# Kernel tuning notes

Hardware: AMD Instinct MI355X
Metric: run time of the kernel (lower is better)

## Reference

```python
import jax, jax.numpy as jnp
import numpy as np

B, T, I, R, O = 128, 512, 64, 512, 64

def setup_inputs() -> dict:
    key = jax.random.key(0)
    ks = jax.random.split(key, 6)
    s = lambda fan_in: 1.0 / np.sqrt(fan_in)
    return {
        "x_pred": jax.random.normal(ks[0], (B, T, I), dtype=jnp.float32),
        "h0": jnp.zeros((B, R), dtype=jnp.float32),
        "W_h": jax.random.uniform(ks[1], (R, R), jnp.float32, -s(R), s(R)),
        "b_h": jax.random.uniform(ks[2], (R,), jnp.float32, -s(R), s(R)),
        "U_h": jax.random.uniform(ks[3], (R, I), jnp.float32, -s(I), s(I)),
        "W_out": jax.random.uniform(ks[4], (O, R), jnp.float32, -s(R), s(R)),
        "b_out": jax.random.uniform(ks[5], (O,), jnp.float32, -s(R), s(R)),
    }

def reference(x_pred, h0, W_h, b_h, U_h, W_out, b_out):
    # Precompute input projections for all timesteps: [T, B, R]
    u = jnp.einsum('bti,ri->tbr', x_pred, U_h)

    def step(x, u_t):
        # x: [B, R] hidden state; u_t: [B, R]
        x = jnp.tanh(x @ W_h.T + b_h + u_t)
        y_t = x @ W_out.T + b_out  # [B, O]
        return x, y_t

    x_last, y = jax.lax.scan(step, h0, u)
    y = jnp.transpose(y, (1, 0, 2))  # [B, T, O]
    return y, (x_last, x_last)
```

## Files before the change

### kernel.cpp

```cpp
#include <hip/hip_runtime.h>

#define B_ 128
#define T_ 512
#define I_ 64
#define R_ 512
#define O_ 64
#define NG 8
#define GB 16

typedef _Float16 f16;
typedef __attribute__((ext_vector_type(8))) _Float16 half8;
typedef __attribute__((ext_vector_type(2))) __fp16 fp16x2;
typedef __attribute__((ext_vector_type(4))) float f32x4;

#define MFMA16 __builtin_amdgcn_mfma_f32_16x16x32_f16

#define NLW 15
#define NRW 49
#define WLDS_BYTES (8 * NLW * 1024)
#define HOFF WLDS_BYTES
#define HBYTES 16384
#define SMEM_TOTAL (WLDS_BYTES + 2 * HBYTES)

__device__ __forceinline__ float tanh_fast(float x) {
    float e = __builtin_amdgcn_exp2f(x * 2.885390081777927f);
    return 1.0f - 2.0f * __builtin_amdgcn_rcpf(e + 1.0f);
}

__device__ __forceinline__ half8 cvt_h8(const float4 a, const float4 b) {
    half8 r;
    r[0] = (f16)a.x; r[1] = (f16)a.y; r[2] = (f16)a.z; r[3] = (f16)a.w;
    r[4] = (f16)b.x; r[5] = (f16)b.y; r[6] = (f16)b.z; r[7] = (f16)b.w;
    return r;
}

__device__ __forceinline__ unsigned pack2(float a, float b) {
    union { fp16x2 h; unsigned u; } r;
    r.h = __builtin_amdgcn_cvt_pkrtz(a, b);
    return r.u;
}

__global__ void __launch_bounds__(256) pre_kernel(
    const float* __restrict__ x_pred, const float* __restrict__ b_h,
    const float* __restrict__ U_h, f16* __restrict__ ubuf)
{
    const int tid = threadIdx.x;
    const int w = tid >> 6, l = tid & 63, lg = l >> 4, ln = l & 15;
    const int g = blockIdx.x & 7, tc = blockIdx.x >> 3;
    const int b0 = g * GB;

    half8 uf[8][2];
    float4 bh4[8];
    #pragma unroll
    for (int j = 0; j < 8; ++j) {
        const int rt = 128 * w + 16 * j;
        bh4[j] = *(const float4*)(b_h + rt + 4 * lg);
        #pragma unroll
        for (int ks = 0; ks < 2; ++ks) {
            const float* p = U_h + (size_t)(rt + ln) * I_ + 32 * ks + 8 * lg;
            uf[j][ks] = cvt_h8(*(const float4*)p, *(const float4*)(p + 4));
        }
    }
    for (int tt = 0; tt < 4; ++tt) {
        const int t = tc * 4 + tt;
        half8 xf[2];
        #pragma unroll
        for (int ks = 0; ks < 2; ++ks) {
            const float* p = x_pred + ((size_t)(b0 + ln) * T_ + t) * I_ + 32 * ks + 8 * lg;
            xf[ks] = cvt_h8(*(const float4*)p, *(const float4*)(p + 4));
        }
        char* ut = (char*)ubuf + (size_t)(t * NG + g) * 16384;
        #pragma unroll
        for (int j = 0; j < 8; ++j) {
            f32x4 acc = {0.f, 0.f, 0.f, 0.f};
            acc = MFMA16(uf[j][0], xf[0], acc, 0, 0, 0);
            acc = MFMA16(uf[j][1], xf[1], acc, 0, 0, 0);
            const int rt = 128 * w + 16 * j;
            uint2 pk;
            pk.x = pack2(acc[0] + bh4[j].x, acc[1] + bh4[j].y);
            pk.y = pack2(acc[2] + bh4[j].z, acc[3] + bh4[j].w);
            *(uint2*)(ut + ln * 1024 + 2 * (rt + 4 * lg)) = pk;
        }
    }
}

__global__ void __launch_bounds__(512, 2) rnn_kernel(
    const float* __restrict__ h0, const float* __restrict__ W_h,
    f16* __restrict__ uh, float* __restrict__ out)
{
    extern __shared__ char smem[];
    const int tid = threadIdx.x;
    const int w = tid >> 6, l = tid & 63, lg = l >> 4, ln = l & 15;
    const int g = blockIdx.x;
    const int b0 = g * GB;
    const int rw = w * 64;
    char* wlds = smem + ((w * NLW) << 10) + (l << 4);

    half8 wfr[NRW];
    #pragma unroll
    for (int j = 0; j < 4; ++j) {
        const float* wr = W_h + (size_t)(rw + 16 * j + ln) * R_;
        #pragma unroll
        for (int ks = 0; ks < 16; ++ks) {
            const float* p = wr + 32 * ks + 8 * lg;
            half8 f = cvt_h8(*(const float4*)p, *(const float4*)(p + 4));
            const int fi = ks * 4 + j;
            if (fi < NLW) *(half8*)(wlds + (fi << 10)) = f;
            else wfr[fi - NLW] = f;
        }
    }
    {
        const int b = tid >> 5, r0 = (tid & 31) * 16;
        const int sb = (b & 7) << 4;
        const float* hp = h0 + (size_t)(b0 + b) * R_ + r0;
        #pragma unroll
        for (int q = 0; q < 4; ++q) {
            float4 v = *(const float4*)(hp + 4 * q);
            uint2 pk;
            pk.x = pack2(v.x, v.y); pk.y = pack2(v.z, v.w);
            *(uint2*)(smem + HOFF + b * 1024 + ((2 * (r0 + 4 * q)) ^ sb)) = pk;
        }
    }
    uint2 uu[4];
    #pragma unroll
    for (int j = 0; j < 4; ++j)
        uu[j] = *(const uint2*)((char*)uh + (size_t)g * 16384 + ln * 1024 + 2 * (rw + 16 * j + 4 * lg));
    __syncthreads();

    const int asb = (ln & 7) << 4;
    const unsigned lanebase = (unsigned)(ln * 1024)
                            + (((unsigned)(16 * lg)) ^ ((unsigned)(ln & 3) << 4))
                            + (((unsigned)(ln >> 2) & 1u) << 6);

    #pragma unroll 1
    for (int t = 0; t < T_; ++t) {
        char* hc = smem + HOFF + (t & 1) * HBYTES;
        char* hn = smem + HOFF + ((t & 1) ^ 1) * HBYTES;
        const char* hbE = hc + lanebase;
        const char* hbO = hc + (lanebase ^ 64u);
        char* slot = (char*)uh + (size_t)(t * NG + g) * 16384;
        const bool lastt = (t == T_ - 1);

        f32x4 acc[4];
        #pragma unroll
        for (int j = 0; j < 4; ++j) {
            union { uint2 u; f16 h[4]; } c; c.u = uu[j];
            acc[j] = (f32x4){(float)c.h[0], (float)c.h[1], (float)c.h[2], (float)c.h[3]};
        }
        if (!lastt) {
            const char* un = (const char*)uh + (size_t)((t + 1) * NG + g) * 16384;
            #pragma unroll
            for (int j = 0; j < 4; ++j)
                uu[j] = *(const uint2*)(un + ln * 1024 + 2 * (rw + 16 * j + 4 * lg));
        }
        __builtin_amdgcn_s_setprio(1);
        #pragma unroll
        for (int ks = 0; ks < 16; ++ks) {
            half8 hb = *(const half8*)((ks & 1 ? hbO : hbE) + 128 * (ks >> 1));
            #pragma unroll
            for (int j = 0; j < 4; ++j) {
                const int fi = ks * 4 + j;
                half8 aa;
                if (fi < NLW) aa = *(const half8*)(wlds + (fi << 10));
                else aa = wfr[fi - NLW];
                acc[j] = MFMA16(aa, hb, acc[j], 0, 0, 0);
            }
        }
        __builtin_amdgcn_s_setprio(0);
        #pragma unroll
        for (int j = 0; j < 4; ++j) {
            const int rb = 2 * (rw + 16 * j + 4 * lg);
            float v0 = tanh_fast(acc[j][0]), v1 = tanh_fast(acc[j][1]);
            float v2 = tanh_fast(acc[j][2]), v3 = tanh_fast(acc[j][3]);
            uint2 pk;
            pk.x = pack2(v0, v1); pk.y = pack2(v2, v3);
            if (!lastt) {
                *(uint2*)(hn + ln * 1024 + (rb ^ asb)) = pk;
                *(uint2*)(slot + ln * 1024 + rb) = pk;
            } else {
                *(uint2*)(slot + ln * 1024 + rb) = pk;
                float* xd = out + (size_t)B_ * T_ * O_ + (size_t)(b0 + ln) * R_ + (rw + 16 * j + 4 * lg);
                float4 xv = make_float4(v0, v1, v2, v3);
                *(float4*)xd = xv;
                *(float4*)(xd + (size_t)B_ * R_) = xv;
            }
        }
        asm volatile("s_waitcnt lgkmcnt(0)\n\ts_barrier" ::: "memory");
    }
}

__global__ void __launch_bounds__(256) y_kernel(
    const f16* __restrict__ hbuf, const float* __restrict__ W_out,
    const float* __restrict__ b_out, float* __restrict__ out)
{
    const int tid = threadIdx.x;
    const int w = tid >> 6, l = tid & 63, lg = l >> 4, ln = l & 15;
    const int g = blockIdx.x & 7, tc = blockIdx.x >> 3;
    const int b0 = g * GB;

    half8 wf[16];
    #pragma unroll
    for (int ks = 0; ks < 16; ++ks) {
        const float* p = W_out + (size_t)(16 * w + ln) * R_ + 32 * ks + 8 * lg;
        wf[ks] = cvt_h8(*(const float4*)p, *(const float4*)(p + 4));
    }
    const float bo = b_out[16 * w + ln];

    for (int tt = 0; tt < 4; ++tt) {
        const int t = tc * 4 + tt;
        const char* hb = (const char*)hbuf + (size_t)(t * NG + g) * 16384;
        f32x4 acc = {0.f, 0.f, 0.f, 0.f};
        #pragma unroll
        for (int ks = 0; ks < 16; ++ks) {
            half8 a = *(const half8*)(hb + ln * 1024 + 64 * ks + 16 * lg);
            acc = MFMA16(a, wf[ks], acc, 0, 0, 0);
        }
        #pragma unroll
        for (int q = 0; q < 4; ++q) {
            const int b = 4 * lg + q;
            out[((size_t)(b0 + b) * T_ + t) * O_ + 16 * w + ln] = acc[q] + bo;
        }
    }
}

extern "C" void kernel_launch(void* const* d_in, const int* in_sizes, int n_in,
                              void* d_out, int out_size, void* d_ws, size_t ws_size,
                              hipStream_t stream) {
    const float* x_pred = (const float*)d_in[0];
    const float* h0     = (const float*)d_in[1];
    const float* W_h    = (const float*)d_in[2];
    const float* b_h    = (const float*)d_in[3];
    const float* U_h    = (const float*)d_in[4];
    const float* W_out  = (const float*)d_in[5];
    const float* b_out  = (const float*)d_in[6];
    float* out = (float*)d_out;

    f16* ubuf = (f16*)d_ws;

    (void)hipFuncSetAttribute(reinterpret_cast<const void*>(rnn_kernel),
                              hipFuncAttributeMaxDynamicSharedMemorySize, SMEM_TOTAL);

    pre_kernel<<<dim3(NG * 128), dim3(256), 0, stream>>>(x_pred, b_h, U_h, ubuf);
    rnn_kernel<<<dim3(NG), dim3(512), SMEM_TOTAL, stream>>>(h0, W_h, ubuf, out);
    y_kernel<<<dim3(NG * 128), dim3(256), 0, stream>>>(ubuf, W_out, b_out, out);
}
```

Baseline: 1.761 ms.

## Stream spilled W_h fragments from global scratch instead of LDS

```diff
diff --git a/kernel.cpp b/kernel.cpp
--- a/kernel.cpp
+++ b/kernel.cpp
@@ -15,12 +15,9 @@
 
 #define MFMA16 __builtin_amdgcn_mfma_f32_16x16x32_f16
 
-#define NLW 15
-#define NRW 49
-#define WLDS_BYTES (8 * NLW * 1024)
-#define HOFF WLDS_BYTES
+#define HOFF 0
 #define HBYTES 16384
-#define SMEM_TOTAL (WLDS_BYTES + 2 * HBYTES)
+#define SMEM_TOTAL (2 * HBYTES)
 
 __device__ __forceinline__ float tanh_fast(float x) {
     float e = __builtin_amdgcn_exp2f(x * 2.885390081777927f);
@@ -94,19 +91,17 @@
     const int g = blockIdx.x;
     const int b0 = g * GB;
     const int rw = w * 64;
-    char* wlds = smem + ((w * NLW) << 10) + (l << 4);
-
-    half8 wfr[NRW];
-    #pragma unroll
-    for (int j = 0; j < 4; ++j) {
-        const float* wr = W_h + (size_t)(rw + 16 * j + ln) * R_;
-        #pragma unroll
-        for (int ks = 0; ks < 16; ++ks) {
-            const float* p = wr + 32 * ks + 8 * lg;
+    char* wsbase = (char*)out + ((size_t)(g * 8 + w) << 14) + (l << 4);
+
+    half8 wfr[48];
+    #pragma unroll
+    for (int ks = 0; ks < 16; ++ks) {
+        #pragma unroll
+        for (int j = 0; j < 4; ++j) {
+            const float* p = W_h + (size_t)(rw + 16 * j + ln) * R_ + 32 * ks + 8 * lg;
             half8 f = cvt_h8(*(const float4*)p, *(const float4*)(p + 4));
-            const int fi = ks * 4 + j;
-            if (fi < NLW) *(half8*)(wlds + (fi << 10)) = f;
-            else wfr[fi - NLW] = f;
+            if (j == 3) *(half8*)(wsbase + (ks << 10)) = f;
+            else wfr[ks * 3 + j] = f;
         }
     }
     {
@@ -125,6 +120,7 @@
     #pragma unroll
     for (int j = 0; j < 4; ++j)
         uu[j] = *(const uint2*)((char*)uh + (size_t)g * 16384 + ln * 1024 + 2 * (rw + 16 * j + 4 * lg));
+    asm volatile("s_waitcnt vmcnt(0)" ::: "memory");
     __syncthreads();
 
     const int asb = (ln & 7) << 4;
@@ -153,18 +149,18 @@
             for (int j = 0; j < 4; ++j)
                 uu[j] = *(const uint2*)(un + ln * 1024 + 2 * (rw + 16 * j + 4 * lg));
         }
+        half8 wg[4];
+        #pragma unroll
+        for (int k = 0; k < 4; ++k) wg[k] = *(const half8*)(wsbase + (k << 10));
         __builtin_amdgcn_s_setprio(1);
         #pragma unroll
         for (int ks = 0; ks < 16; ++ks) {
             half8 hb = *(const half8*)((ks & 1 ? hbO : hbE) + 128 * (ks >> 1));
-            #pragma unroll
-            for (int j = 0; j < 4; ++j) {
-                const int fi = ks * 4 + j;
-                half8 aa;
-                if (fi < NLW) aa = *(const half8*)(wlds + (fi << 10));
-                else aa = wfr[fi - NLW];
-                acc[j] = MFMA16(aa, hb, acc[j], 0, 0, 0);
-            }
+            acc[0] = MFMA16(wfr[ks * 3 + 0], hb, acc[0], 0, 0, 0);
+            acc[1] = MFMA16(wfr[ks * 3 + 1], hb, acc[1], 0, 0, 0);
+            acc[2] = MFMA16(wfr[ks * 3 + 2], hb, acc[2], 0, 0, 0);
+            acc[3] = MFMA16(wg[ks & 3], hb, acc[3], 0, 0, 0);
+            if (ks < 12) wg[ks & 3] = *(const half8*)(wsbase + ((ks + 4) << 10));
         }
         __builtin_amdgcn_s_setprio(0);
         #pragma unroll
```

Result: slower. 3.039 ms (+72.6%).
